# Kernel optimization log

Hardware: AMD Instinct MI355X
Metric: run time of the kernel (lower is better)

## Reference

```python
import jax, jax.numpy as jnp
import numpy as np

B, L, E, H = 2, 2048, 1024, 16
D = E // H  # head dim = 64


def setup_inputs() -> dict:
    key = jax.random.key(0)
    ks = jax.random.split(key, 10)
    s = 0.02
    return {
        "xt": jax.random.normal(ks[0], (B, L, E), jnp.float32),
        "xs": jax.random.normal(ks[1], (B, L, E), jnp.float32),
        "Wt": jax.random.normal(ks[2], (E, 3 * E), jnp.float32) * s,  # t_attn weight (x @ Wt)
        "bt": jnp.zeros((3 * E,), jnp.float32),
        "Ws": jax.random.normal(ks[3], (E, 2 * E), jnp.float32) * s,  # s_attn weight
        "bs": jnp.zeros((2 * E,), jnp.float32),
        "Wc": jax.random.normal(ks[4], (E, E), jnp.float32) * s,      # c_proj weight
        "bc": jnp.zeros((E,), jnp.float32),
        "lam_ts": jnp.ones((1,), jnp.float32),
        "lam_st": jnp.ones((1,), jnp.float32),
        "lam_ss": jnp.ones((1,), jnp.float32),
    }


def _heads(x):
    # (B, L, E) -> (B, H, L, D)
    return x.reshape(B, L, H, D).transpose(0, 2, 1, 3)


def reference(xt, xs, Wt, bt, Ws, bs, Wc, bc, lam_ts, lam_st, lam_ss):
    qt, kt, vt = jnp.split(xt @ Wt + bt, 3, axis=2)
    qs, ks = jnp.split(xs @ Ws + bs, 2, axis=2)
    qt, kt, vt, qs, ks = map(_heads, (qt, kt, vt, qs, ks))

    # 4-way disentangled scores; fuse the 4 matmuls into 2 by combining keys:
    # qt@kt^T + lam_ts*qt@ks^T = qt @ (kt + lam_ts*ks)^T
    # lam_st*qs@kt^T + lam_ss*qs@ks^T = qs @ (lam_st*kt + lam_ss*ks)^T
    k1 = kt + lam_ts[0] * ks
    k2 = lam_st[0] * kt + lam_ss[0] * ks
    att = (jnp.einsum('bhqd,bhkd->bhqk', qt, k1)
           + jnp.einsum('bhqd,bhkd->bhqk', qs, k2)) * (1.0 / np.sqrt(D))
    att = jax.nn.softmax(att, axis=-1)
    y = jnp.einsum('bhqk,bhkd->bhqd', att, vt)  # (B, H, L, D)
    y = y.transpose(0, 2, 1, 3).reshape(B, L, E)
    return y @ Wc + bc
```

## Files before the change

### kernel.cpp

```cpp
#include <hip/hip_runtime.h>
#include <math.h>

#define LQ 2048
#define EQ 1024
#define M_ROWS 4096
#define BH 32

typedef _Float16 f16x8 __attribute__((ext_vector_type(8)));
typedef _Float16 f16x4 __attribute__((ext_vector_type(4)));
typedef float f32x4 __attribute__((ext_vector_type(4)));

__device__ __forceinline__ void async_ld16(const _Float16* g, _Float16* l) {
  __builtin_amdgcn_global_load_lds(
      (const __attribute__((address_space(1))) unsigned int*)g,
      (__attribute__((address_space(3))) unsigned int*)l, 16, 0, 0);
}

__global__ __launch_bounds__(256) void convert_x(
    const float* __restrict__ xt, const float* __restrict__ xs,
    _Float16* __restrict__ xt16, _Float16* __restrict__ xs16) {
  int i = blockIdx.x * 256 + threadIdx.x;
  const float* s; _Float16* d; size_t off;
  if (i < 524288) { s = xt; d = xt16; off = (size_t)i * 8; }
  else            { s = xs; d = xs16; off = (size_t)(i - 524288) * 8; }
  float4 a = *(const float4*)&s[off];
  float4 b = *(const float4*)&s[off + 4];
  f16x8 h;
  h[0] = (_Float16)a.x; h[1] = (_Float16)a.y; h[2] = (_Float16)a.z; h[3] = (_Float16)a.w;
  h[4] = (_Float16)b.x; h[5] = (_Float16)b.y; h[6] = (_Float16)b.z; h[7] = (_Float16)b.w;
  *(f16x8*)&d[off] = h;
}

__global__ __launch_bounds__(256) void transpose_w(
    const float* __restrict__ Wt, const float* __restrict__ Ws,
    const float* __restrict__ Wc,
    _Float16* __restrict__ WtT, _Float16* __restrict__ WsT,
    _Float16* __restrict__ WcT) {
  __shared__ float T[32][33];
  int tx = threadIdx.x & 31, ty = threadIdx.x >> 5;
  int c0 = blockIdx.x * 32;
  int k0 = blockIdx.y * 32;
  const float* W; _Float16* D; int Nw, cl;
  if (c0 < 3072)      { W = Wt; D = WtT; Nw = 3072; cl = c0; }
  else if (c0 < 5120) { W = Ws; D = WsT; Nw = 2048; cl = c0 - 3072; }
  else                { W = Wc; D = WcT; Nw = 1024; cl = c0 - 5120; }
#pragma unroll
  for (int j = 0; j < 4; ++j)
    T[ty + j * 8][tx] = W[(size_t)(k0 + ty + j * 8) * Nw + cl + tx];
  __syncthreads();
#pragma unroll
  for (int j = 0; j < 4; ++j)
    D[(size_t)(cl + ty + j * 8) * 1024 + k0 + tx] = (_Float16)T[tx][ty + j * 8];
}

__global__ __launch_bounds__(256) void gemm_bt(
    const _Float16* __restrict__ A, const _Float16* __restrict__ Bm,
    const float* __restrict__ bias,
    float* __restrict__ outf, _Float16* __restrict__ q16,
    _Float16* __restrict__ k16, _Float16* __restrict__ v16,
    int N, int mode) {
  __shared__ _Float16 Al[128 * 32];
  __shared__ _Float16 Bl[128 * 32];

  const int tid = threadIdx.x;
  const int w = tid >> 6;
  const int lane = tid & 63;
  const int quad = lane >> 4;
  const int l15 = lane & 15;
  const int wm = w >> 1, wn = w & 1;
  const int m0 = blockIdx.y * 128;
  const int n0 = blockIdx.x * 128;

  const int srow = lane >> 2;
  const int schunk = ((lane & 3) ^ ((lane >> 3) & 3)) * 8;

  f32x4 acc[4][4];
#pragma unroll
  for (int mb = 0; mb < 4; ++mb)
#pragma unroll
    for (int nb = 0; nb < 4; ++nb) acc[mb][nb] = (f32x4){0.f, 0.f, 0.f, 0.f};

  const int key = (l15 >> 1) & 3;

  for (int kt = 0; kt < 1024; kt += 32) {
    __syncthreads();
#pragma unroll
    for (int i = 0; i < 2; ++i) {
      int rt = w * 32 + i * 16;
      async_ld16(&A[(size_t)(m0 + rt + srow) * 1024 + kt + schunk], &Al[rt * 32]);
      async_ld16(&Bm[(size_t)(n0 + rt + srow) * 1024 + kt + schunk], &Bl[rt * 32]);
    }
    __syncthreads();

    f16x8 af[4], bf[4];
    const int pc = (quad ^ key) * 8;
#pragma unroll
    for (int mb = 0; mb < 4; ++mb)
      af[mb] = *(f16x8*)&Al[(wm * 64 + mb * 16 + l15) * 32 + pc];
#pragma unroll
    for (int nb = 0; nb < 4; ++nb)
      bf[nb] = *(f16x8*)&Bl[(wn * 64 + nb * 16 + l15) * 32 + pc];
#pragma unroll
    for (int mb = 0; mb < 4; ++mb)
#pragma unroll
      for (int nb = 0; nb < 4; ++nb)
        acc[mb][nb] = __builtin_amdgcn_mfma_f32_16x16x32_f16(af[mb], bf[nb], acc[mb][nb], 0, 0, 0);
  }

#pragma unroll
  for (int mb = 0; mb < 4; ++mb)
#pragma unroll
    for (int nb = 0; nb < 4; ++nb)
#pragma unroll
      for (int r = 0; r < 4; ++r) {
        int row = m0 + wm * 64 + mb * 16 + quad * 4 + r;
        int col = n0 + wn * 64 + nb * 16 + l15;
        float val = acc[mb][nb][r] + bias[col];
        if (mode == 2) {
          outf[(size_t)row * 1024 + col] = val;
        } else {
          int bb = row >> 11, ll = row & 2047;
          int which = col >> 10, e = col & 1023;
          int hh = e >> 6, dd = e & 63;
          size_t rowhd = (size_t)(bb * 16 + hh) * 2048 + ll;
          if (mode == 0) {
            if (which == 0)      q16[rowhd * 128 + dd] = (_Float16)(val * 0.125f);
            else if (which == 1) k16[rowhd * 128 + dd] = (_Float16)val;
            else                 v16[rowhd * 64 + dd] = (_Float16)val;
          } else {
            if (which == 0) q16[rowhd * 128 + 64 + dd] = (_Float16)(val * 0.125f);
            else            k16[rowhd * 128 + 64 + dd] = (_Float16)val;
          }
        }
      }
}

__global__ __launch_bounds__(256) void combine16(
    _Float16* __restrict__ kcat, const float* __restrict__ lam_ts,
    const float* __restrict__ lam_st, const float* __restrict__ lam_ss) {
  int idx = blockIdx.x * 256 + threadIdx.x;
  int row = idx >> 3;
  int d8 = (idx & 7) * 8;
  float lts = lam_ts[0], lst = lam_st[0], lss = lam_ss[0];
  size_t base = (size_t)row * 128;
  f16x8 a = *(f16x8*)&kcat[base + d8];
  f16x8 b = *(f16x8*)&kcat[base + 64 + d8];
  f16x8 o1, o2;
#pragma unroll
  for (int e = 0; e < 8; ++e) {
    float kt = (float)a[e], ks = (float)b[e];
    o1[e] = (_Float16)(kt + lts * ks);
    o2[e] = (_Float16)(lst * kt + lss * ks);
  }
  *(f16x8*)&kcat[base + d8] = o1;
  *(f16x8*)&kcat[base + 64 + d8] = o2;
}

__global__ __launch_bounds__(256) void flash_attn_mfma(
    const _Float16* __restrict__ qcat, const _Float16* __restrict__ kcat,
    const _Float16* __restrict__ v, _Float16* __restrict__ y) {
  const int bh = blockIdx.y;
  const int qt0 = blockIdx.x * 128;
  const int b = bh >> 4, h = bh & 15;
  const _Float16* Qg = qcat + (size_t)bh * LQ * 128;
  const _Float16* Kg = kcat + (size_t)bh * LQ * 128;
  const _Float16* Vg = v + (size_t)bh * LQ * 64;

  __shared__ _Float16 Ksh[64 * 136];
  __shared__ _Float16 Vt[64 * 72];
  __shared__ _Float16 Psh[4 * 32 * 72];

  const int tid = threadIdx.x;
  const int w = tid >> 6;
  const int lane = tid & 63;
  const int quad = lane >> 4;
  const int l15 = lane & 15;

  f16x8 qf[2][4];
#pragma unroll
  for (int qb = 0; qb < 2; ++qb)
#pragma unroll
    for (int db = 0; db < 4; ++db)
      qf[qb][db] = *(const f16x8*)&Qg[(size_t)(qt0 + w * 32 + qb * 16 + l15) * 128 + db * 32 + quad * 8];

  float m_i[2] = {-INFINITY, -INFINITY};
  float l_i[2] = {0.f, 0.f};
  f32x4 O[2][4];
#pragma unroll
  for (int mb = 0; mb < 2; ++mb)
#pragma unroll
    for (int nb = 0; nb < 4; ++nb) O[mb][nb] = (f32x4){0.f, 0.f, 0.f, 0.f};

  _Float16* Pw = &Psh[w * 32 * 72];

  for (int t = 0; t < LQ; t += 64) {
    __syncthreads();

#pragma unroll
    for (int p = 0; p < 4; ++p) {
      int idx = p * 256 + tid;
      int row = idx >> 4;
      int c8 = (idx & 15) * 8;
      *(f16x8*)&Ksh[row * 136 + c8] = *(const f16x8*)&Kg[(size_t)(t + row) * 128 + c8];
    }
#pragma unroll
    for (int p = 0; p < 2; ++p) {
      int d8 = (p * 4 + w) * 8;
      f16x8 vv = *(const f16x8*)&Vg[(size_t)(t + lane) * 64 + d8];
#pragma unroll
      for (int e = 0; e < 8; ++e) Vt[(d8 + e) * 72 + lane] = vv[e];
    }
    __syncthreads();

    f32x4 S[4][2];
#pragma unroll
    for (int kb = 0; kb < 4; ++kb)
#pragma unroll
      for (int qb = 0; qb < 2; ++qb) S[kb][qb] = (f32x4){0.f, 0.f, 0.f, 0.f};

#pragma unroll
    for (int db = 0; db < 4; ++db) {
      f16x8 af[4];
#pragma unroll
      for (int kb = 0; kb < 4; ++kb)
        af[kb] = *(f16x8*)&Ksh[(kb * 16 + l15) * 136 + db * 32 + quad * 8];
#pragma unroll
      for (int kb = 0; kb < 4; ++kb)
#pragma unroll
        for (int qb = 0; qb < 2; ++qb)
          S[kb][qb] = __builtin_amdgcn_mfma_f32_16x16x32_f16(af[kb], qf[qb][db], S[kb][qb], 0, 0, 0);
    }

    float alpha[2];
#pragma unroll
    for (int qb = 0; qb < 2; ++qb) {
      float mx = -INFINITY;
#pragma unroll
      for (int kb = 0; kb < 4; ++kb)
#pragma unroll
        for (int r = 0; r < 4; ++r) mx = fmaxf(mx, S[kb][qb][r]);
      mx = fmaxf(mx, __shfl_xor(mx, 16));
      mx = fmaxf(mx, __shfl_xor(mx, 32));
      float m_new = fmaxf(m_i[qb], mx);
      alpha[qb] = __expf(m_i[qb] - m_new);
      float s = 0.f;
#pragma unroll
      for (int kb = 0; kb < 4; ++kb)
#pragma unroll
        for (int r = 0; r < 4; ++r) {
          float p = __expf(S[kb][qb][r] - m_new);
          S[kb][qb][r] = p;
          s += p;
        }
      s += __shfl_xor(s, 16);
      s += __shfl_xor(s, 32);
      l_i[qb] = l_i[qb] * alpha[qb] + s;
      m_i[qb] = m_new;
    }

#pragma unroll
    for (int qb = 0; qb < 2; ++qb)
#pragma unroll
      for (int kb = 0; kb < 4; ++kb) {
        f16x4 p4;
        p4[0] = (_Float16)S[kb][qb][0];
        p4[1] = (_Float16)S[kb][qb][1];
        p4[2] = (_Float16)S[kb][qb][2];
        p4[3] = (_Float16)S[kb][qb][3];
        *(f16x4*)&Pw[(qb * 16 + l15) * 72 + kb * 16 + quad * 4] = p4;
      }

#pragma unroll
    for (int mb = 0; mb < 2; ++mb)
#pragma unroll
      for (int r = 0; r < 4; ++r) {
        float ab = __shfl(alpha[mb], quad * 4 + r);
#pragma unroll
        for (int nb = 0; nb < 4; ++nb) O[mb][nb][r] *= ab;
      }

#pragma unroll
    for (int kb2 = 0; kb2 < 2; ++kb2) {
      f16x8 ap[2], bv[4];
#pragma unroll
      for (int mb = 0; mb < 2; ++mb)
        ap[mb] = *(f16x8*)&Pw[(mb * 16 + l15) * 72 + kb2 * 32 + quad * 8];
#pragma unroll
      for (int nb = 0; nb < 4; ++nb)
        bv[nb] = *(f16x8*)&Vt[(nb * 16 + l15) * 72 + kb2 * 32 + quad * 8];
#pragma unroll
      for (int mb = 0; mb < 2; ++mb)
#pragma unroll
        for (int nb = 0; nb < 4; ++nb)
          O[mb][nb] = __builtin_amdgcn_mfma_f32_16x16x32_f16(ap[mb], bv[nb], O[mb][nb], 0, 0, 0);
    }
  }

#pragma unroll
  for (int mb = 0; mb < 2; ++mb)
#pragma unroll
    for (int r = 0; r < 4; ++r) {
      float li = __shfl(l_i[mb], quad * 4 + r);
      float inv = 1.f / li;
      int qrow = qt0 + w * 32 + mb * 16 + quad * 4 + r;
#pragma unroll
      for (int nb = 0; nb < 4; ++nb)
        y[((size_t)b * LQ + qrow) * EQ + h * 64 + nb * 16 + l15] = (_Float16)(O[mb][nb][r] * inv);
    }
}

extern "C" void kernel_launch(void* const* d_in, const int* in_sizes, int n_in,
                              void* d_out, int out_size, void* d_ws, size_t ws_size,
                              hipStream_t stream) {
  const float* xt = (const float*)d_in[0];
  const float* xs = (const float*)d_in[1];
  const float* Wt = (const float*)d_in[2];
  const float* bt = (const float*)d_in[3];
  const float* Ws = (const float*)d_in[4];
  const float* bs = (const float*)d_in[5];
  const float* Wc = (const float*)d_in[6];
  const float* bc = (const float*)d_in[7];
  const float* lam_ts = (const float*)d_in[8];
  const float* lam_st = (const float*)d_in[9];
  const float* lam_ss = (const float*)d_in[10];
  float* out = (float*)d_out;

  _Float16* w16 = (_Float16*)d_ws;
  _Float16* xt16 = w16;
  _Float16* xs16 = xt16 + 4194304;
  _Float16* WtT  = xs16 + 4194304;
  _Float16* WsT  = WtT + 3145728;
  _Float16* WcT  = WsT + 2097152;
  _Float16* qcat = WcT + 1048576;
  _Float16* kcat = qcat + 8388608;
  _Float16* vbuf = kcat + 8388608;
  _Float16* ybuf = vbuf + 4194304;

  convert_x<<<4096, 256, 0, stream>>>(xt, xs, xt16, xs16);
  transpose_w<<<dim3(192, 32), 256, 0, stream>>>(Wt, Ws, Wc, WtT, WsT, WcT);
  gemm_bt<<<dim3(24, 32), 256, 0, stream>>>(
      xt16, WtT, bt, nullptr, qcat, kcat, vbuf, 3072, 0);
  gemm_bt<<<dim3(16, 32), 256, 0, stream>>>(
      xs16, WsT, bs, nullptr, qcat, kcat, nullptr, 2048, 1);
  combine16<<<2048, 256, 0, stream>>>(kcat, lam_ts, lam_st, lam_ss);
  flash_attn_mfma<<<dim3(16, 32), 256, 0, stream>>>(qcat, kcat, vbuf, ybuf);
  gemm_bt<<<dim3(8, 32), 256, 0, stream>>>(
      ybuf, WcT, bc, out, nullptr, nullptr, nullptr, 1024, 2);
}
```

Measured before the change: 314.2 us.

## Restructure flash attention to 8 waves with async swizzled K loads and exp2

The attention kernel now runs 512 threads per block, with each wave owning 16 query rows instead of 32. K tiles are loaded with global_load_lds into an XOR-swizzled unpadded layout rather than through registers. V is register-prefetched one tile ahead. The softmax uses exp2, with log2(e) folded into the Q scale. These changes aim to cut register pressure, hide load latency and remove LDS bank conflicts, at the cost of more waves contending for barriers and less Q reuse per wave.

```diff
diff --git a/kernel.cpp b/kernel.cpp
--- a/kernel.cpp
+++ b/kernel.cpp
@@ -9,6 +9,8 @@
 typedef _Float16 f16x8 __attribute__((ext_vector_type(8)));
 typedef _Float16 f16x4 __attribute__((ext_vector_type(4)));
 typedef float f32x4 __attribute__((ext_vector_type(4)));
+
+#define QSCALE 0.1803368801111204f
 
 __device__ __forceinline__ void async_ld16(const _Float16* g, _Float16* l) {
   __builtin_amdgcn_global_load_lds(
@@ -124,11 +126,11 @@
           int hh = e >> 6, dd = e & 63;
           size_t rowhd = (size_t)(bb * 16 + hh) * 2048 + ll;
           if (mode == 0) {
-            if (which == 0)      q16[rowhd * 128 + dd] = (_Float16)(val * 0.125f);
+            if (which == 0)      q16[rowhd * 128 + dd] = (_Float16)(val * QSCALE);
             else if (which == 1) k16[rowhd * 128 + dd] = (_Float16)val;
             else                 v16[rowhd * 64 + dd] = (_Float16)val;
           } else {
-            if (which == 0) q16[rowhd * 128 + 64 + dd] = (_Float16)(val * 0.125f);
+            if (which == 0) q16[rowhd * 128 + 64 + dd] = (_Float16)(val * QSCALE);
             else            k16[rowhd * 128 + 64 + dd] = (_Float16)val;
           }
         }
@@ -156,7 +158,7 @@
   *(f16x8*)&kcat[base + 64 + d8] = o2;
 }
 
-__global__ __launch_bounds__(256) void flash_attn_mfma(
+__global__ __launch_bounds__(512, 4) void flash_attn_mfma(
     const _Float16* __restrict__ qcat, const _Float16* __restrict__ kcat,
     const _Float16* __restrict__ v, _Float16* __restrict__ y) {
   const int bh = blockIdx.y;
@@ -166,9 +168,9 @@
   const _Float16* Kg = kcat + (size_t)bh * LQ * 128;
   const _Float16* Vg = v + (size_t)bh * LQ * 64;
 
-  __shared__ _Float16 Ksh[64 * 136];
+  __shared__ _Float16 Ksh[64 * 128];
   __shared__ _Float16 Vt[64 * 72];
-  __shared__ _Float16 Psh[4 * 32 * 72];
+  __shared__ _Float16 Psh[8 * 16 * 72];
 
   const int tid = threadIdx.x;
   const int w = tid >> 6;
@@ -176,137 +178,119 @@
   const int quad = lane >> 4;
   const int l15 = lane & 15;
 
-  f16x8 qf[2][4];
-#pragma unroll
-  for (int qb = 0; qb < 2; ++qb)
-#pragma unroll
-    for (int db = 0; db < 4; ++db)
-      qf[qb][db] = *(const f16x8*)&Qg[(size_t)(qt0 + w * 32 + qb * 16 + l15) * 128 + db * 32 + quad * 8];
-
-  float m_i[2] = {-INFINITY, -INFINITY};
-  float l_i[2] = {0.f, 0.f};
-  f32x4 O[2][4];
-#pragma unroll
-  for (int mb = 0; mb < 2; ++mb)
-#pragma unroll
-    for (int nb = 0; nb < 4; ++nb) O[mb][nb] = (f32x4){0.f, 0.f, 0.f, 0.f};
-
-  _Float16* Pw = &Psh[w * 32 * 72];
+  f16x8 qf[4];
+#pragma unroll
+  for (int db = 0; db < 4; ++db)
+    qf[db] = *(const f16x8*)&Qg[(size_t)(qt0 + w * 16 + l15) * 128 + db * 32 + quad * 8];
+
+  float m_i = -INFINITY;
+  float l_i = 0.f;
+  f32x4 O[4];
+#pragma unroll
+  for (int nb = 0; nb < 4; ++nb) O[nb] = (f32x4){0.f, 0.f, 0.f, 0.f};
+
+  _Float16* Pw = &Psh[w * 16 * 72];
+
+  int krow[2], kgc[2];
+#pragma unroll
+  for (int a = 0; a < 2; ++a) {
+    krow[a] = w * 8 + a * 4 + (lane >> 4);
+    kgc[a] = (lane & 15) ^ (krow[a] & 7);
+  }
+  const _Float16* vsrc = Vg + (size_t)lane * 64 + w * 8;
+  f16x8 vv = *(const f16x8*)vsrc;
 
   for (int t = 0; t < LQ; t += 64) {
     __syncthreads();
 
 #pragma unroll
-    for (int p = 0; p < 4; ++p) {
-      int idx = p * 256 + tid;
-      int row = idx >> 4;
-      int c8 = (idx & 15) * 8;
-      *(f16x8*)&Ksh[row * 136 + c8] = *(const f16x8*)&Kg[(size_t)(t + row) * 128 + c8];
-    }
-#pragma unroll
-    for (int p = 0; p < 2; ++p) {
-      int d8 = (p * 4 + w) * 8;
-      f16x8 vv = *(const f16x8*)&Vg[(size_t)(t + lane) * 64 + d8];
-#pragma unroll
-      for (int e = 0; e < 8; ++e) Vt[(d8 + e) * 72 + lane] = vv[e];
-    }
+    for (int a = 0; a < 2; ++a)
+      async_ld16(&Kg[(size_t)(t + krow[a]) * 128 + kgc[a] * 8],
+                 &Ksh[(w * 8 + a * 4) * 128]);
+
+#pragma unroll
+    for (int e = 0; e < 8; ++e) Vt[(w * 8 + e) * 72 + lane] = vv[e];
+    if (t + 64 < LQ) vv = *(const f16x8*)(vsrc + (size_t)(t + 64) * 64);
+
     __syncthreads();
 
-    f32x4 S[4][2];
+    f32x4 S[4];
+#pragma unroll
+    for (int kb = 0; kb < 4; ++kb) S[kb] = (f32x4){0.f, 0.f, 0.f, 0.f};
+#pragma unroll
+    for (int db = 0; db < 4; ++db) {
+      const int pc = ((db * 4 + quad) ^ (l15 & 7)) * 8;
+      f16x8 af[4];
+#pragma unroll
+      for (int kb = 0; kb < 4; ++kb)
+        af[kb] = *(f16x8*)&Ksh[(kb * 16 + l15) * 128 + pc];
+#pragma unroll
+      for (int kb = 0; kb < 4; ++kb)
+        S[kb] = __builtin_amdgcn_mfma_f32_16x16x32_f16(af[kb], qf[db], S[kb], 0, 0, 0);
+    }
+
+    float mx = -INFINITY;
 #pragma unroll
     for (int kb = 0; kb < 4; ++kb)
 #pragma unroll
-      for (int qb = 0; qb < 2; ++qb) S[kb][qb] = (f32x4){0.f, 0.f, 0.f, 0.f};
-
-#pragma unroll
-    for (int db = 0; db < 4; ++db) {
-      f16x8 af[4];
-#pragma unroll
-      for (int kb = 0; kb < 4; ++kb)
-        af[kb] = *(f16x8*)&Ksh[(kb * 16 + l15) * 136 + db * 32 + quad * 8];
-#pragma unroll
-      for (int kb = 0; kb < 4; ++kb)
-#pragma unroll
-        for (int qb = 0; qb < 2; ++qb)
-          S[kb][qb] = __builtin_amdgcn_mfma_f32_16x16x32_f16(af[kb], qf[qb][db], S[kb][qb], 0, 0, 0);
-    }
-
-    float alpha[2];
-#pragma unroll
-    for (int qb = 0; qb < 2; ++qb) {
-      float mx = -INFINITY;
-#pragma unroll
-      for (int kb = 0; kb < 4; ++kb)
-#pragma unroll
-        for (int r = 0; r < 4; ++r) mx = fmaxf(mx, S[kb][qb][r]);
-      mx = fmaxf(mx, __shfl_xor(mx, 16));
-      mx = fmaxf(mx, __shfl_xor(mx, 32));
-      float m_new = fmaxf(m_i[qb], mx);
-      alpha[qb] = __expf(m_i[qb] - m_new);
-      float s = 0.f;
-#pragma unroll
-      for (int kb = 0; kb < 4; ++kb)
-#pragma unroll
-        for (int r = 0; r < 4; ++r) {
-          float p = __expf(S[kb][qb][r] - m_new);
-          S[kb][qb][r] = p;
-          s += p;
-        }
-      s += __shfl_xor(s, 16);
-      s += __shfl_xor(s, 32);
-      l_i[qb] = l_i[qb] * alpha[qb] + s;
-      m_i[qb] = m_new;
-    }
-
-#pragma unroll
-    for (int qb = 0; qb < 2; ++qb)
-#pragma unroll
-      for (int kb = 0; kb < 4; ++kb) {
-        f16x4 p4;
-        p4[0] = (_Float16)S[kb][qb][0];
-        p4[1] = (_Float16)S[kb][qb][1];
-        p4[2] = (_Float16)S[kb][qb][2];
-        p4[3] = (_Float16)S[kb][qb][3];
-        *(f16x4*)&Pw[(qb * 16 + l15) * 72 + kb * 16 + quad * 4] = p4;
+      for (int r = 0; r < 4; ++r) mx = fmaxf(mx, S[kb][r]);
+    mx = fmaxf(mx, __shfl_xor(mx, 16));
+    mx = fmaxf(mx, __shfl_xor(mx, 32));
+    float m_new = fmaxf(m_i, mx);
+    float alpha = __builtin_amdgcn_exp2f(m_i - m_new);
+    float s = 0.f;
+#pragma unroll
+    for (int kb = 0; kb < 4; ++kb)
+#pragma unroll
+      for (int r = 0; r < 4; ++r) {
+        float p = __builtin_amdgcn_exp2f(S[kb][r] - m_new);
+        S[kb][r] = p;
+        s += p;
       }
-
-#pragma unroll
-    for (int mb = 0; mb < 2; ++mb)
-#pragma unroll
-      for (int r = 0; r < 4; ++r) {
-        float ab = __shfl(alpha[mb], quad * 4 + r);
-#pragma unroll
-        for (int nb = 0; nb < 4; ++nb) O[mb][nb][r] *= ab;
-      }
+    s += __shfl_xor(s, 16);
+    s += __shfl_xor(s, 32);
+    l_i = l_i * alpha + s;
+    m_i = m_new;
+
+#pragma unroll
+    for (int kb = 0; kb < 4; ++kb) {
+      f16x4 p4;
+      p4[0] = (_Float16)S[kb][0];
+      p4[1] = (_Float16)S[kb][1];
+      p4[2] = (_Float16)S[kb][2];
+      p4[3] = (_Float16)S[kb][3];
+      *(f16x4*)&Pw[l15 * 72 + kb * 16 + quad * 4] = p4;
+    }
+
+#pragma unroll
+    for (int r = 0; r < 4; ++r) {
+      float ab = __shfl(alpha, quad * 4 + r);
+#pragma unroll
+      for (int nb = 0; nb < 4; ++nb) O[nb][r] *= ab;
+    }
 
 #pragma unroll
     for (int kb2 = 0; kb2 < 2; ++kb2) {
-      f16x8 ap[2], bv[4];
-#pragma unroll
-      for (int mb = 0; mb < 2; ++mb)
-        ap[mb] = *(f16x8*)&Pw[(mb * 16 + l15) * 72 + kb2 * 32 + quad * 8];
+      f16x8 ap = *(f16x8*)&Pw[l15 * 72 + kb2 * 32 + quad * 8];
+      f16x8 bv[4];
 #pragma unroll
       for (int nb = 0; nb < 4; ++nb)
         bv[nb] = *(f16x8*)&Vt[(nb * 16 + l15) * 72 + kb2 * 32 + quad * 8];
 #pragma unroll
-      for (int mb = 0; mb < 2; ++mb)
-#pragma unroll
-        for (int nb = 0; nb < 4; ++nb)
-          O[mb][nb] = __builtin_amdgcn_mfma_f32_16x16x32_f16(ap[mb], bv[nb], O[mb][nb], 0, 0, 0);
-    }
-  }
-
-#pragma unroll
-  for (int mb = 0; mb < 2; ++mb)
-#pragma unroll
-    for (int r = 0; r < 4; ++r) {
-      float li = __shfl(l_i[mb], quad * 4 + r);
-      float inv = 1.f / li;
-      int qrow = qt0 + w * 32 + mb * 16 + quad * 4 + r;
-#pragma unroll
       for (int nb = 0; nb < 4; ++nb)
-        y[((size_t)b * LQ + qrow) * EQ + h * 64 + nb * 16 + l15] = (_Float16)(O[mb][nb][r] * inv);
-    }
+        O[nb] = __builtin_amdgcn_mfma_f32_16x16x32_f16(ap, bv[nb], O[nb], 0, 0, 0);
+    }
+  }
+
+#pragma unroll
+  for (int r = 0; r < 4; ++r) {
+    float li = __shfl(l_i, quad * 4 + r);
+    float inv = 1.f / li;
+    int qrow = qt0 + w * 16 + quad * 4 + r;
+#pragma unroll
+    for (int nb = 0; nb < 4; ++nb)
+      y[((size_t)b * LQ + qrow) * EQ + h * 64 + nb * 16 + l15] = (_Float16)(O[nb][r] * inv);
+  }
 }
 
 extern "C" void kernel_launch(void* const* d_in, const int* in_sizes, int n_in,
@@ -343,7 +327,7 @@
   gemm_bt<<<dim3(16, 32), 256, 0, stream>>>(
       xs16, WsT, bs, nullptr, qcat, kcat, nullptr, 2048, 1);
   combine16<<<2048, 256, 0, stream>>>(kcat, lam_ts, lam_st, lam_ss);
-  flash_attn_mfma<<<dim3(16, 32), 256, 0, stream>>>(qcat, kcat, vbuf, ybuf);
+  flash_attn_mfma<<<dim3(16, 32), 512, 0, stream>>>(qcat, kcat, vbuf, ybuf);
   gemm_bt<<<dim3(8, 32), 256, 0, stream>>>(
       ybuf, WcT, bc, out, nullptr, nullptr, nullptr, 1024, 2);
 }
```

Measured after the change: 304.7 us. 1.03x faster.
